# Performance work log

Measured on AMD Instinct MI355X. Metric: run time of the kernel, lower is better.

## Reference

```python
import jax, jax.numpy as jnp
import numpy as np

N = 50000      # nodes
E = 800000     # edges (before self-loops)
F_IN = 256     # num_features
H = 8          # heads (conv1)
C = 32         # hidden_size per head (conv1)
OUT = 2        # conv2 out channels (1 head)
NEG_SLOPE = 0.2


def setup_inputs() -> dict:
    key = jax.random.key(0)
    ks = jax.random.split(key, 12)
    x = jax.random.normal(ks[0], (N, F_IN), jnp.float32)
    edge_index = jax.random.randint(ks[1], (2, E), 0, N, dtype=jnp.int64)

    def glorot(k, shape):
        fan = shape[0] if len(shape) == 2 else int(np.prod(shape))
        s = float(np.sqrt(6.0 / (fan + shape[-1])))
        return jax.random.uniform(k, shape, jnp.float32, -s, s)

    W1 = glorot(ks[2], (F_IN, H * C))
    att_src1 = glorot(ks[3], (H, C))
    att_dst1 = glorot(ks[4], (H, C))
    b1 = jnp.zeros((H * C,), jnp.float32)
    W2 = glorot(ks[5], (H * C, 1 * OUT))
    att_src2 = glorot(ks[6], (1, OUT))
    att_dst2 = glorot(ks[7], (1, OUT))
    b2 = jnp.zeros((OUT,), jnp.float32)
    return {"x": x, "edge_index": edge_index, "W1": W1, "att_src1": att_src1,
            "att_dst1": att_dst1, "b1": b1, "W2": W2, "att_src2": att_src2,
            "att_dst2": att_dst2, "b2": b2}


def gat_conv(x, src, dst, W, a_src, a_dst, b, heads, ch, n):
    # x: [n, f] -> projected [n, heads, ch]
    xp = (x @ W).reshape(n, heads, ch)
    alpha_src = jnp.einsum('nhc,hc->nh', xp, a_src)   # [n, H]
    alpha_dst = jnp.einsum('nhc,hc->nh', xp, a_dst)   # [n, H]
    e = jax.nn.leaky_relu(alpha_src[src] + alpha_dst[dst], NEG_SLOPE)  # [E', H]
    # segment softmax over edges grouped by destination node
    m = jax.ops.segment_max(e, dst, num_segments=n)                    # [n, H]
    p = jnp.exp(e - m[dst])
    denom = jax.ops.segment_sum(p, dst, num_segments=n)                # [n, H]
    alpha = p / denom[dst]                                             # [E', H]
    # weighted scatter-aggregate of source messages
    out = jax.ops.segment_sum(xp[src] * alpha[:, :, None], dst, num_segments=n)
    return out.reshape(n, heads * ch) + b


def reference(x, edge_index, W1, att_src1, att_dst1, b1, W2, att_src2, att_dst2, b2):
    n = x.shape[0]
    loops = jnp.arange(n, dtype=edge_index.dtype)  # GATConv add_self_loops=True
    src = jnp.concatenate([edge_index[0], loops])
    dst = jnp.concatenate([edge_index[1], loops])
    h = jax.nn.relu(gat_conv(x, src, dst, W1, att_src1, att_dst1, b1, H, C, n))
    # eval mode: F.dropout and attention dropout are identity
    return gat_conv(h, src, dst, W2, att_src2, att_dst2, b2, 1, OUT, n)
```

## Files before the change

### kernel.cpp

```cpp
#include <hip/hip_runtime.h>
#include <math.h>

#define N_NODES 50000
#define N_EDGES 800000
#define EP (N_EDGES + N_NODES)
#define NEG 0.2f
#define SCAN_BLOCKS 49

typedef __attribute__((ext_vector_type(8))) short bf16x8;
typedef __attribute__((ext_vector_type(4))) float f32x4;

static __device__ __forceinline__ unsigned short bf16_rn(float f) {
    union { float f; unsigned int u; } v; v.f = f;
    unsigned int u = v.u;
    unsigned int r = (u + 0x7FFFu + ((u >> 16) & 1u)) >> 16;
    return (unsigned short)r;
}
static __device__ __forceinline__ float bf16_tof(unsigned short u) {
    union { unsigned int u; float f; } v; v.u = ((unsigned int)u) << 16;
    return v.f;
}


__global__ void k_hist(const int* __restrict__ ei, int* __restrict__ counts) {
    int e = blockIdx.x * 256 + threadIdx.x;
    if (e >= EP) return;
    int d = (e < N_EDGES) ? ei[N_EDGES + e] : (e - N_EDGES);
    atomicAdd(&counts[d], 1);
}

__global__ void k_scan_block(const int* __restrict__ counts, int* __restrict__ excl,
                             int* __restrict__ bsums) {
    __shared__ int wsum[4];
    int b = blockIdx.x, t = threadIdx.x;
    int lane = t & 63, w = t >> 6;
    int i0 = b * 1024 + t * 4;
    int v0 = (i0 + 0 < N_NODES) ? counts[i0 + 0] : 0;
    int v1 = (i0 + 1 < N_NODES) ? counts[i0 + 1] : 0;
    int v2 = (i0 + 2 < N_NODES) ? counts[i0 + 2] : 0;
    int v3 = (i0 + 3 < N_NODES) ? counts[i0 + 3] : 0;
    int s = v0 + v1 + v2 + v3;
    int incl = s;
    #pragma unroll
    for (int d = 1; d < 64; d <<= 1) {
        int u = __shfl_up(incl, d);
        if (lane >= d) incl += u;
    }
    if (lane == 63) wsum[w] = incl;
    __syncthreads();
    if (t == 0) {
        int run = 0;
        #pragma unroll
        for (int i = 0; i < 4; ++i) { int x = wsum[i]; wsum[i] = run; run += x; }
        bsums[b] = run;
    }
    __syncthreads();
    int base = wsum[w] + incl - s;
    if (i0 + 0 < N_NODES) excl[i0 + 0] = base;
    if (i0 + 1 < N_NODES) excl[i0 + 1] = base + v0;
    if (i0 + 2 < N_NODES) excl[i0 + 2] = base + v0 + v1;
    if (i0 + 3 < N_NODES) excl[i0 + 3] = base + v0 + v1 + v2;
}

__global__ void k_scan_mid(int* __restrict__ bsums) {
    int t = threadIdx.x;
    int v = (t < SCAN_BLOCKS) ? bsums[t] : 0;
    int incl = v;
    #pragma unroll
    for (int d = 1; d < 64; d <<= 1) {
        int u = __shfl_up(incl, d);
        if (t >= d) incl += u;
    }
    if (t < SCAN_BLOCKS) bsums[t] = incl - v;
}

__global__ void k_scan_add(int* __restrict__ row_ptr, const int* __restrict__ bsums) {
    int b = blockIdx.x, t = threadIdx.x;
    int off = bsums[b];
    int i0 = b * 1024 + t * 4;
    #pragma unroll
    for (int j = 0; j < 4; ++j)
        if (i0 + j < N_NODES) row_ptr[i0 + j] += off;
    if (b == 0 && t == 0) row_ptr[N_NODES] = EP;
}

__global__ void k_scatter(const int* __restrict__ ei, const int* __restrict__ row_ptr,
                          int* __restrict__ fill, int* __restrict__ colb) {
    int e = blockIdx.x * 256 + threadIdx.x;
    if (e >= EP) return;
    int s, d;
    if (e < N_EDGES) { s = ei[e]; d = ei[N_EDGES + e]; }
    else             { s = e - N_EDGES; d = s; }
    int pos = row_ptr[d] + atomicAdd(&fill[d], 1);
    colb[pos] = s;
}

__global__ void k_cvtW(const float* __restrict__ W1, unsigned short* __restrict__ Wt) {
    int c = blockIdx.x;
    int k = threadIdx.x;
    Wt[c * 256 + k] = bf16_rn(W1[k * 256 + c]);
}

#define GM_GRID 782
__global__ __launch_bounds__(256) void
k_gemm1m(const float* __restrict__ x, const unsigned short* __restrict__ Wt,
         unsigned short* __restrict__ xp1b) {
    int t = threadIdx.x, l = t & 63, w = t >> 6;
    int rowbase = blockIdx.x * 64 + w * 16;
    int m = l & 15, kg = l >> 4;

    f32x4 acc[16];
    #pragma unroll
    for (int nt = 0; nt < 16; ++nt) acc[nt] = (f32x4){0.f, 0.f, 0.f, 0.f};

    int gra = rowbase + m;
    if (gra > N_NODES - 1) gra = N_NODES - 1;
    const float4* x4 = (const float4*)x;
    const bf16x8* WtV = (const bf16x8*)Wt;

    #pragma unroll 2
    for (int c = 0; c < 8; ++c) {
        int k0 = c * 32;
        int fi = (gra * 256 + k0 + kg * 8) >> 2;
        float4 xa = x4[fi];
        float4 xb = x4[fi + 1];
        bf16x8 aF;
        aF[0] = (short)bf16_rn(xa.x); aF[1] = (short)bf16_rn(xa.y);
        aF[2] = (short)bf16_rn(xa.z); aF[3] = (short)bf16_rn(xa.w);
        aF[4] = (short)bf16_rn(xb.x); aF[5] = (short)bf16_rn(xb.y);
        aF[6] = (short)bf16_rn(xb.z); aF[7] = (short)bf16_rn(xb.w);
        #pragma unroll
        for (int nt = 0; nt < 16; ++nt) {
            bf16x8 bF = WtV[(nt * 16 + m) * 32 + c * 4 + kg];
            acc[nt] = __builtin_amdgcn_mfma_f32_16x16x32_bf16(aF, bF, acc[nt], 0, 0, 0);
        }
    }

    int cbase = l & 15, rq = l >> 4;
    #pragma unroll
    for (int reg = 0; reg < 4; ++reg) {
        int gr = rowbase + rq * 4 + reg;
        if (gr < N_NODES) {
            #pragma unroll
            for (int nt = 0; nt < 16; ++nt)
                xp1b[gr * 256 + nt * 16 + cbase] = bf16_rn(acc[nt][reg]);
        }
    }
}

__global__ void k_alphas1(const ushort4* __restrict__ xpb, const float* __restrict__ asrc,
                          const float* __restrict__ adst,
                          float* __restrict__ as1, float* __restrict__ ad1) {
    int t = threadIdx.x, l = t & 63, w = t >> 6;
    int n = blockIdx.x * 4 + w;
    ushort4 xq = xpb[n * 64 + l];
    float x0 = bf16_tof(xq.x), x1 = bf16_tof(xq.y), x2 = bf16_tof(xq.z), x3 = bf16_tof(xq.w);
    float4 a_s = ((const float4*)asrc)[l];
    float4 a_d = ((const float4*)adst)[l];
    float ds = x0 * a_s.x + x1 * a_s.y + x2 * a_s.z + x3 * a_s.w;
    float dd = x0 * a_d.x + x1 * a_d.y + x2 * a_d.z + x3 * a_d.w;
    #pragma unroll
    for (int m = 1; m < 8; m <<= 1) {
        ds += __shfl_xor(ds, m);
        dd += __shfl_xor(dd, m);
    }
    if ((l & 7) == 0) {
        int h = l >> 3;
        as1[n * 8 + h] = ds;
        ad1[n * 8 + h] = dd;
    }
}

__global__ void k_agg1(const ushort4* __restrict__ xpb, const float* __restrict__ as1,
                       const float* __restrict__ ad1, const int* __restrict__ row_ptr,
                       const int* __restrict__ colb, const float* __restrict__ b1,
                       const float* __restrict__ W2, const float* __restrict__ as2w,
                       const float* __restrict__ ad2w,
                       float* __restrict__ xp2, float* __restrict__ as2,
                       float* __restrict__ ad2) {
    int t = threadIdx.x, l = t & 63, w = t >> 6;
    int n = blockIdx.x * 4 + w;
    int hidx = l >> 3;
    float adn = ad1[n * 8 + hidx];
    int start = row_ptr[n], end = row_ptr[n + 1];
    float4 acc = {0.f, 0.f, 0.f, 0.f};
    float den = 0.f;
    int j = start;
    for (; j + 4 <= end; j += 4) {
        int s0 = colb[j], s1 = colb[j + 1], s2 = colb[j + 2], s3 = colb[j + 3];
        ushort4 x0 = xpb[s0 * 64 + l];
        ushort4 x1 = xpb[s1 * 64 + l];
        ushort4 x2 = xpb[s2 * 64 + l];
        ushort4 x3 = xpb[s3 * 64 + l];
        float e0 = as1[s0 * 8 + hidx] + adn;
        float e1 = as1[s1 * 8 + hidx] + adn;
        float e2 = as1[s2 * 8 + hidx] + adn;
        float e3 = as1[s3 * 8 + hidx] + adn;
        e0 = (e0 > 0.f) ? e0 : NEG * e0;
        e1 = (e1 > 0.f) ? e1 : NEG * e1;
        e2 = (e2 > 0.f) ? e2 : NEG * e2;
        e3 = (e3 > 0.f) ? e3 : NEG * e3;
        float p0 = __expf(e0), p1 = __expf(e1), p2 = __expf(e2), p3 = __expf(e3);
        den += (p0 + p1) + (p2 + p3);
        acc.x = fmaf(p0, bf16_tof(x0.x), acc.x);
        acc.y = fmaf(p0, bf16_tof(x0.y), acc.y);
        acc.z = fmaf(p0, bf16_tof(x0.z), acc.z);
        acc.w = fmaf(p0, bf16_tof(x0.w), acc.w);
        acc.x = fmaf(p1, bf16_tof(x1.x), acc.x);
        acc.y = fmaf(p1, bf16_tof(x1.y), acc.y);
        acc.z = fmaf(p1, bf16_tof(x1.z), acc.z);
        acc.w = fmaf(p1, bf16_tof(x1.w), acc.w);
        acc.x = fmaf(p2, bf16_tof(x2.x), acc.x);
        acc.y = fmaf(p2, bf16_tof(x2.y), acc.y);
        acc.z = fmaf(p2, bf16_tof(x2.z), acc.z);
        acc.w = fmaf(p2, bf16_tof(x2.w), acc.w);
        acc.x = fmaf(p3, bf16_tof(x3.x), acc.x);
        acc.y = fmaf(p3, bf16_tof(x3.y), acc.y);
        acc.z = fmaf(p3, bf16_tof(x3.z), acc.z);
        acc.w = fmaf(p3, bf16_tof(x3.w), acc.w);
    }
    for (; j < end; ++j) {
        int s = colb[j];
        ushort4 xv = xpb[s * 64 + l];
        float e = as1[s * 8 + hidx] + adn;
        e = (e > 0.f) ? e : NEG * e;
        float p = __expf(e);
        den += p;
        acc.x = fmaf(p, bf16_tof(xv.x), acc.x);
        acc.y = fmaf(p, bf16_tof(xv.y), acc.y);
        acc.z = fmaf(p, bf16_tof(xv.z), acc.z);
        acc.w = fmaf(p, bf16_tof(xv.w), acc.w);
    }
    float4 bv = ((const float4*)b1)[l];
    float inv = 1.f / den;
    float4 o;
    o.x = fmaxf(acc.x * inv + bv.x, 0.f);
    o.y = fmaxf(acc.y * inv + bv.y, 0.f);
    o.z = fmaxf(acc.z * inv + bv.z, 0.f);
    o.w = fmaxf(acc.w * inv + bv.w, 0.f);
    float4 wa = ((const float4*)W2)[2 * l];
    float4 wb = ((const float4*)W2)[2 * l + 1];
    float d0 = o.x * wa.x + o.y * wa.z + o.z * wb.x + o.w * wb.z;
    float d1 = o.x * wa.y + o.y * wa.w + o.z * wb.y + o.w * wb.w;
    #pragma unroll
    for (int m = 1; m < 64; m <<= 1) {
        d0 += __shfl_xor(d0, m);
        d1 += __shfl_xor(d1, m);
    }
    if (l == 0) {
        xp2[2 * n] = d0;
        xp2[2 * n + 1] = d1;
        as2[n] = d0 * as2w[0] + d1 * as2w[1];
        ad2[n] = d0 * ad2w[0] + d1 * ad2w[1];
    }
}

__global__ void k_agg2(const float* __restrict__ xp2, const float* __restrict__ as2,
                       const float* __restrict__ ad2, const int* __restrict__ row_ptr,
                       const int* __restrict__ colb, const float* __restrict__ b2,
                       float* __restrict__ out) {
    int t = threadIdx.x, l = t & 63, w = t >> 6;
    int n = blockIdx.x * 4 + w;
    int start = row_ptr[n], end = row_ptr[n + 1];
    float adn = ad2[n];
    float a0 = 0.f, a1 = 0.f, den = 0.f;
    for (int j = start + l; j < end; j += 64) {
        int s = colb[j];
        float e = as2[s] + adn;
        e = (e > 0.f) ? e : NEG * e;
        float p = __expf(e);
        den += p;
        a0 = fmaf(p, xp2[2 * s], a0);
        a1 = fmaf(p, xp2[2 * s + 1], a1);
    }
    #pragma unroll
    for (int m = 1; m < 64; m <<= 1) {
        a0 += __shfl_xor(a0, m);
        a1 += __shfl_xor(a1, m);
        den += __shfl_xor(den, m);
    }
    if (l == 0) {
        out[2 * n] = a0 / den + b2[0];
        out[2 * n + 1] = a1 / den + b2[1];
    }
}

extern "C" void kernel_launch(void* const* d_in, const int* in_sizes, int n_in,
                              void* d_out, int out_size, void* d_ws, size_t ws_size,
                              hipStream_t stream) {
    const float* x     = (const float*)d_in[0];
    const int*   ei    = (const int*)d_in[1];
    const float* W1    = (const float*)d_in[2];
    const float* asrc1 = (const float*)d_in[3];
    const float* adst1 = (const float*)d_in[4];
    const float* b1    = (const float*)d_in[5];
    const float* W2    = (const float*)d_in[6];
    const float* asrc2 = (const float*)d_in[7];
    const float* adst2 = (const float*)d_in[8];
    const float* b2    = (const float*)d_in[9];
    float* out = (float*)d_out;

    char* ws = (char*)d_ws;
    unsigned short* xp1b = (unsigned short*)(ws + 0);
    unsigned short* Wt   = (unsigned short*)(ws + 25600000);
    float* as1     = (float*)(ws + 102400000);
    float* ad1     = (float*)(ws + 104000000);
    float* xp2     = (float*)(ws + 105600000);
    float* as2     = (float*)(ws + 106000000);
    float* ad2     = (float*)(ws + 106200000);
    int*   counts  = (int*)  (ws + 106400000);
    int*   fill    = (int*)  (ws + 106600000);
    int*   row_ptr = (int*)  (ws + 106800000);
    int*   colb    = (int*)  (ws + 107000064);
    int*   bsums   = (int*)  (ws + 110400064);

    hipMemsetAsync(counts, 0, 400000, stream);

    int egrid = (EP + 255) / 256;
    k_hist      <<<egrid,       256, 0, stream>>>(ei, counts);
    k_scan_block<<<SCAN_BLOCKS, 256, 0, stream>>>(counts, row_ptr, bsums);
    k_scan_mid  <<<1,            64, 0, stream>>>(bsums);
    k_scan_add  <<<SCAN_BLOCKS, 256, 0, stream>>>(row_ptr, bsums);
    k_scatter   <<<egrid,       256, 0, stream>>>(ei, row_ptr, fill, colb);

    k_cvtW      <<<256,    256, 0, stream>>>(W1, Wt);
    k_gemm1m    <<<GM_GRID, 256, 0, stream>>>(x, Wt, xp1b);
    k_alphas1   <<<12500,  256, 0, stream>>>((const ushort4*)xp1b, asrc1, adst1, as1, ad1);
    k_agg1      <<<12500,  256, 0, stream>>>((const ushort4*)xp1b, as1, ad1, row_ptr, colb,
                                             b1, W2, asrc2, adst2, xp2, as2, ad2);
    k_agg2      <<<12500,  256, 0, stream>>>(xp2, as2, ad2, row_ptr, colb, b2, out);
}
```

Measured before the change: 347.6 us.

## Pre-swizzle W1 into MFMA fragments, stage in LDS, two row tiles per wave

W1 is now converted once into bf16 MFMA fragment order, so each lane's B operand is one contiguous 16-byte vector. The GEMM kernel stages each 32-wide K slice of those fragments in LDS, shared by the block, instead of every wave reading W from global memory. Each wave now computes two 16-row tiles that reuse each B fragment, and blocks shrink to 128 threads while still covering 64 rows. In exchange, register use doubles to 32 accumulators, which may lower occupancy, and two barriers per K step are added. The GEMM is only one part of the whole pipeline.

```diff
diff --git a/kernel.cpp b/kernel.cpp
--- a/kernel.cpp
+++ b/kernel.cpp
@@ -95,55 +95,84 @@
     colb[pos] = s;
 }
 
-__global__ void k_cvtW(const float* __restrict__ W1, unsigned short* __restrict__ Wt) {
-    int c = blockIdx.x;
-    int k = threadIdx.x;
-    Wt[c * 256 + k] = bf16_rn(W1[k * 256 + c]);
+__global__ void k_cvtWfrag(const float* __restrict__ W1, bf16x8* __restrict__ Wfrag) {
+    int ft = blockIdx.x * 256 + threadIdx.x;
+    int c = ft >> 10, rem = ft & 1023;
+    int nt = rem >> 6, l = rem & 63;
+    int n = nt * 16 + (l & 15);
+    int k0 = c * 32 + (l >> 4) * 8;
+    bf16x8 f;
+    #pragma unroll
+    for (int j = 0; j < 8; ++j)
+        f[j] = (short)bf16_rn(W1[(k0 + j) * 256 + n]);
+    Wfrag[ft] = f;
 }
 
 #define GM_GRID 782
-__global__ __launch_bounds__(256) void
-k_gemm1m(const float* __restrict__ x, const unsigned short* __restrict__ Wt,
+__global__ __launch_bounds__(128) void
+k_gemm1m(const float* __restrict__ x, const bf16x8* __restrict__ Wfrag,
          unsigned short* __restrict__ xp1b) {
+    __shared__ bf16x8 lds[1024];
     int t = threadIdx.x, l = t & 63, w = t >> 6;
-    int rowbase = blockIdx.x * 64 + w * 16;
+    int rowbase = blockIdx.x * 64 + w * 32;
     int m = l & 15, kg = l >> 4;
 
-    f32x4 acc[16];
-    #pragma unroll
-    for (int nt = 0; nt < 16; ++nt) acc[nt] = (f32x4){0.f, 0.f, 0.f, 0.f};
-
-    int gra = rowbase + m;
-    if (gra > N_NODES - 1) gra = N_NODES - 1;
+    f32x4 acc0[16], acc1[16];
+    #pragma unroll
+    for (int nt = 0; nt < 16; ++nt) {
+        acc0[nt] = (f32x4){0.f, 0.f, 0.f, 0.f};
+        acc1[nt] = (f32x4){0.f, 0.f, 0.f, 0.f};
+    }
+
+    int r0 = rowbase + m;
+    int r1 = rowbase + 16 + m;
+    if (r0 > N_NODES - 1) r0 = N_NODES - 1;
+    if (r1 > N_NODES - 1) r1 = N_NODES - 1;
     const float4* x4 = (const float4*)x;
-    const bf16x8* WtV = (const bf16x8*)Wt;
-
-    #pragma unroll 2
+
     for (int c = 0; c < 8; ++c) {
-        int k0 = c * 32;
-        int fi = (gra * 256 + k0 + kg * 8) >> 2;
-        float4 xa = x4[fi];
-        float4 xb = x4[fi + 1];
-        bf16x8 aF;
-        aF[0] = (short)bf16_rn(xa.x); aF[1] = (short)bf16_rn(xa.y);
-        aF[2] = (short)bf16_rn(xa.z); aF[3] = (short)bf16_rn(xa.w);
-        aF[4] = (short)bf16_rn(xb.x); aF[5] = (short)bf16_rn(xb.y);
-        aF[6] = (short)bf16_rn(xb.z); aF[7] = (short)bf16_rn(xb.w);
+        __syncthreads();
+        const bf16x8* src = Wfrag + c * 1024;
+        #pragma unroll
+        for (int q = 0; q < 8; ++q)
+            lds[q * 128 + t] = src[q * 128 + t];
+        __syncthreads();
+
+        int kb = (c * 32 + kg * 8) >> 2;
+        float4 xa0 = x4[r0 * 64 + kb], xb0 = x4[r0 * 64 + kb + 1];
+        float4 xa1 = x4[r1 * 64 + kb], xb1 = x4[r1 * 64 + kb + 1];
+        bf16x8 aF0, aF1;
+        aF0[0] = (short)bf16_rn(xa0.x); aF0[1] = (short)bf16_rn(xa0.y);
+        aF0[2] = (short)bf16_rn(xa0.z); aF0[3] = (short)bf16_rn(xa0.w);
+        aF0[4] = (short)bf16_rn(xb0.x); aF0[5] = (short)bf16_rn(xb0.y);
+        aF0[6] = (short)bf16_rn(xb0.z); aF0[7] = (short)bf16_rn(xb0.w);
+        aF1[0] = (short)bf16_rn(xa1.x); aF1[1] = (short)bf16_rn(xa1.y);
+        aF1[2] = (short)bf16_rn(xa1.z); aF1[3] = (short)bf16_rn(xa1.w);
+        aF1[4] = (short)bf16_rn(xb1.x); aF1[5] = (short)bf16_rn(xb1.y);
+        aF1[6] = (short)bf16_rn(xb1.z); aF1[7] = (short)bf16_rn(xb1.w);
+
         #pragma unroll
         for (int nt = 0; nt < 16; ++nt) {
-            bf16x8 bF = WtV[(nt * 16 + m) * 32 + c * 4 + kg];
-            acc[nt] = __builtin_amdgcn_mfma_f32_16x16x32_bf16(aF, bF, acc[nt], 0, 0, 0);
+            bf16x8 bF = lds[nt * 64 + l];
+            acc0[nt] = __builtin_amdgcn_mfma_f32_16x16x32_bf16(aF0, bF, acc0[nt], 0, 0, 0);
+            acc1[nt] = __builtin_amdgcn_mfma_f32_16x16x32_bf16(aF1, bF, acc1[nt], 0, 0, 0);
         }
     }
 
     int cbase = l & 15, rq = l >> 4;
     #pragma unroll
     for (int reg = 0; reg < 4; ++reg) {
-        int gr = rowbase + rq * 4 + reg;
-        if (gr < N_NODES) {
+        int g0 = rowbase + rq * 4 + reg;
+        int g1 = rowbase + 16 + rq * 4 + reg;
+        if (g0 < N_NODES) {
             #pragma unroll
             for (int nt = 0; nt < 16; ++nt)
-                xp1b[gr * 256 + nt * 16 + cbase] = bf16_rn(acc[nt][reg]);
+                xp1b[g0 * 256 + nt * 16 + cbase] = bf16_rn(acc0[nt][reg]);
+        }
+        if (g1 < N_NODES) {
+            #pragma unroll
+            for (int nt = 0; nt < 16; ++nt)
+                xp1b[g1 * 256 + nt * 16 + cbase] = bf16_rn(acc1[nt][reg]);
         }
     }
 }
@@ -302,7 +331,7 @@
 
     char* ws = (char*)d_ws;
     unsigned short* xp1b = (unsigned short*)(ws + 0);
-    unsigned short* Wt   = (unsigned short*)(ws + 25600000);
+    bf16x8* Wfrag  = (bf16x8*)(ws + 25600000);
     float* as1     = (float*)(ws + 102400000);
     float* ad1     = (float*)(ws + 104000000);
     float* xp2     = (float*)(ws + 105600000);
@@ -323,8 +352,8 @@
     k_scan_add  <<<SCAN_BLOCKS, 256, 0, stream>>>(row_ptr, bsums);
     k_scatter   <<<egrid,       256, 0, stream>>>(ei, row_ptr, fill, colb);
 
-    k_cvtW      <<<256,    256, 0, stream>>>(W1, Wt);
-    k_gemm1m    <<<GM_GRID, 256, 0, stream>>>(x, Wt, xp1b);
+    k_cvtWfrag  <<<32,     256, 0, stream>>>(W1, Wfrag);
+    k_gemm1m    <<<GM_GRID, 128, 0, stream>>>(x, Wfrag, xp1b);
     k_alphas1   <<<12500,  256, 0, stream>>>((const ushort4*)xp1b, asrc1, adst1, as1, ad1);
     k_agg1      <<<12500,  256, 0, stream>>>((const ushort4*)xp1b, as1, ad1, row_ptr, colb,
                                              b1, W2, asrc2, adst2, xp2, as2, ad2);
```

After: 297.5 us. 14.4% less time.
